# Kernel optimization log

Hardware: AMD Instinct MI355X
Metric: run time of the kernel (lower is better)

The kernel has to match this reference:

```python
import jax, jax.numpy as jnp
import numpy as np

BS, P, MAX_GT, C_IN, NCLS = 16, 4096, 32, 512, 4


def _make_boxes(key, shape):
    k1, k2, k3, k4 = jax.random.split(key, 4)
    x0 = jax.random.uniform(k1, shape) * 500.0
    y0 = jax.random.uniform(k2, shape) * 500.0
    w = 10.0 + jax.random.uniform(k3, shape) * 90.0
    h = 10.0 + jax.random.uniform(k4, shape) * 90.0
    return jnp.stack([x0, y0, x0 + w, y0 + h], -1)


def setup_inputs() -> dict:
    key = jax.random.key(0)
    ks = jax.random.split(key, 10)
    v = jax.random.normal(ks[0], (BS * P, C_IN), jnp.float32)
    rois = _make_boxes(ks[1], (BS, P))
    gt_boxes = _make_boxes(ks[2], (BS, MAX_GT))
    gt_counts = jax.random.randint(ks[3], (BS,), 0, MAX_GT + 1, jnp.int32)
    lab_idx = jax.random.randint(ks[4], (BS,), 0, NCLS)
    labels = jax.nn.one_hot(lab_idx, NCLS, dtype=jnp.float32)
    pre_score = jax.random.uniform(ks[5], (BS, P, NCLS), dtype=jnp.float32)
    cls_w = jax.random.normal(ks[6], (NCLS, C_IN), jnp.float32) * 0.01
    cls_b = jnp.full((NCLS,), -np.log((1.0 - 0.01) / 0.01), jnp.float32)
    reg_w = jax.random.normal(ks[7], (NCLS, C_IN), jnp.float32) * 0.01
    reg_b = jnp.zeros((NCLS,), jnp.float32)
    return {"v": v, "gt_boxes": gt_boxes, "gt_counts": gt_counts, "rois": rois,
            "labels": labels, "pre_score": pre_score, "cls_w": cls_w,
            "cls_b": cls_b, "reg_w": reg_w, "reg_b": reg_b}


def _box_iou(a, b):
    # a: (bs, Na, 4), b: (bs, Nb, 4) -> (bs, Na, Nb)
    area_a = (a[..., 2] - a[..., 0]) * (a[..., 3] - a[..., 1])
    area_b = (b[..., 2] - b[..., 0]) * (b[..., 3] - b[..., 1])
    lt = jnp.maximum(a[..., :, None, :2], b[..., None, :, :2])
    rb = jnp.minimum(a[..., :, None, 2:], b[..., None, :, 2:])
    wh = jnp.clip(rb - lt, 0.0)
    inter = wh[..., 0] * wh[..., 1]
    return inter / (area_a[..., :, None] + area_b[..., None, :] - inter)


def _ce(logits, tgt3):
    # CrossEntropyLoss(reduction='none'): logsumexp - logit[target]
    return jax.nn.logsumexp(logits, -1) - jnp.take_along_axis(logits, tgt3, -1)[..., 0]


def _smooth_l1(x):
    ax = jnp.abs(x)
    return jnp.where(ax < 1.0, 0.5 * ax * ax, ax - 0.5)


def reference(v, gt_boxes, gt_counts, rois, labels, pre_score, cls_w, cls_b, reg_w, reg_b):
    bs, Pn = rois.shape[:2]
    classify = (v @ cls_w.T + cls_b).reshape(bs, Pn, NCLS)
    reg = (v @ reg_w.T + reg_b).reshape(bs, Pn, NCLS)
    label = jnp.argmax(labels, 1)                                  # (bs,)
    lbl3 = jnp.broadcast_to(label[:, None, None], (bs, Pn, 1))

    # background branch: CE on raw logits, mean over proposals
    ce_bg = _ce(classify, lbl3).mean(1)                            # (bs,)

    # foreground branch: CE on clamped logits weighted by pre_score
    c = jnp.clip(classify, 1e-7, 1.0 - 1e-7)
    ps = jnp.take_along_axis(pre_score, lbl3, 2)[..., 0]           # (bs, P)
    ce_fg = _ce(c, lbl3) * ps

    gt_valid = jnp.arange(MAX_GT)[None, :] < gt_counts[:, None]    # (bs, MAX_GT)
    ious = _box_iou(gt_boxes, rois)                                # (bs, MAX_GT, P)
    ious = jnp.where(gt_valid[:, :, None], ious, -1.0)
    mask = jnp.any(ious > 0.5, 1).astype(classify.dtype)           # (bs, P)
    c_fg = (ce_fg * mask).sum(1) / (mask.sum(1) + 1e-7)

    idx = jnp.argmax(ious, 1)                                      # (bs, P)
    g = jnp.take_along_axis(gt_boxes, jnp.broadcast_to(idx[:, :, None], (bs, Pn, 4)), 1)
    gx = (g[..., 2] + g[..., 0]) / 2; gy = (g[..., 3] + g[..., 1]) / 2
    gw = (g[..., 2] - g[..., 0]) / 2; gh = (g[..., 3] - g[..., 1]) / 2
    r = rois
    rx = (r[..., 2] + r[..., 0]) / 2; ry = (r[..., 3] + r[..., 1]) / 2
    rw = (r[..., 2] - r[..., 0]) / 2; rh = (r[..., 3] - r[..., 1]) / 2
    tx = (gx - rx) / (rw + 1e-8); ty = (gy - ry) / (rh + 1e-8)
    tw = jnp.log(gw / (rw + 1e-8)); th = jnp.log(gh / (rh + 1e-8))
    t = jnp.stack([tx, ty, tw, th], -1)                            # (bs, P, 4)
    l1 = (_smooth_l1(reg - t).sum(-1) * mask * ps).sum(1) / (bs * Pn)

    has_gt = gt_counts > 0
    c_list = jnp.where(has_gt, c_fg, 0.0).sum()
    c_bg = jnp.where(has_gt, 0.0, ce_bg).sum()
    bg = jnp.where(has_gt, 0.0, float(Pn)).sum()
    l1_list = jnp.where(has_gt, l1, 0.0).sum()
    return (c_list + c_bg / (bg + 1e-7)) / (bs + 1e-7) + l1_list
```

## Files before the change

kernel.cpp:

```cpp
#include <hip/hip_runtime.h>
#include <math.h>

#define BSZ 16
#define NP 4096
#define MAXGT 32
#define CIN 512
#define NCLS 4

__global__ __launch_bounds__(256) void oicr_main(
    const float* __restrict__ v,
    const float* __restrict__ gt_boxes,
    const int*   __restrict__ gt_counts,
    const float* __restrict__ rois,
    const float* __restrict__ labels,
    const float* __restrict__ pre_score,
    const float* __restrict__ cls_w,
    const float* __restrict__ cls_b,
    const float* __restrict__ reg_w,
    const float* __restrict__ reg_b,
    float* __restrict__ partials)
{
    __shared__ float w8[8][CIN];
    __shared__ float s_bias[8];
    __shared__ float g_x0[MAXGT], g_y0[MAXGT], g_x1[MAXGT], g_y1[MAXGT];
    __shared__ float g_area[MAXGT];
    __shared__ int   g_valid[MAXGT];
    __shared__ int   s_label;
    __shared__ float4 red[256];

    const int tid = threadIdx.x;
    const int b   = blockIdx.x >> 4;
    const int p   = ((blockIdx.x & 15) << 8) + tid;
    const int row = b * NP + p;

    for (int i = tid; i < 8 * CIN; i += 256) {
        int c = i >> 9, k = i & (CIN - 1);
        w8[c][k] = (c < 4) ? cls_w[c * CIN + k] : reg_w[(c - 4) * CIN + k];
    }
    if (tid < 8) s_bias[tid] = (tid < 4) ? cls_b[tid] : reg_b[tid - 4];
    if (tid < MAXGT) {
        int cnt = gt_counts[b];
        const float* g = gt_boxes + (size_t)(b * MAXGT + tid) * 4;
        float x0 = g[0], y0 = g[1], x1 = g[2], y1 = g[3];
        g_x0[tid] = x0; g_y0[tid] = y0; g_x1[tid] = x1; g_y1[tid] = y1;
        g_area[tid] = (x1 - x0) * (y1 - y0);
        g_valid[tid] = (tid < cnt) ? 1 : 0;
    }
    if (tid == 0) {
        const float* L = labels + b * NCLS;
        int bi = 0; float bv = L[0];
        #pragma unroll
        for (int c = 1; c < NCLS; ++c) { if (L[c] > bv) { bv = L[c]; bi = c; } }
        s_label = bi;
    }
    __syncthreads();

    float acc[8];
    #pragma unroll
    for (int c = 0; c < 8; ++c) acc[c] = 0.f;

    const float4* vrow = (const float4*)(v + (size_t)row * CIN);
    #pragma unroll 8
    for (int k4 = 0; k4 < CIN / 4; ++k4) {
        float4 a = vrow[k4];
        const int k = k4 * 4;
        #pragma unroll
        for (int c = 0; c < 8; ++c) {
            float4 wv = *(const float4*)&w8[c][k];
            acc[c] += a.x * wv.x + a.y * wv.y + a.z * wv.z + a.w * wv.w;
        }
    }

    const float cls0 = acc[0] + s_bias[0];
    const float cls1 = acc[1] + s_bias[1];
    const float cls2 = acc[2] + s_bias[2];
    const float cls3 = acc[3] + s_bias[3];
    const float reg0 = acc[4] + s_bias[4];
    const float reg1 = acc[5] + s_bias[5];
    const float reg2 = acc[6] + s_bias[6];
    const float reg3 = acc[7] + s_bias[7];

    const int lbl = s_label;

    float mB = fmaxf(fmaxf(cls0, cls1), fmaxf(cls2, cls3));
    float lseB = mB + logf(expf(cls0 - mB) + expf(cls1 - mB) +
                           expf(cls2 - mB) + expf(cls3 - mB));
    float clsL = (lbl == 0) ? cls0 : (lbl == 1) ? cls1 : (lbl == 2) ? cls2 : cls3;
    float ce_bg = lseB - clsL;

    const float lo = 1e-7f, hi = 1.f - 1e-7f;
    float cc0 = fminf(fmaxf(cls0, lo), hi);
    float cc1 = fminf(fmaxf(cls1, lo), hi);
    float cc2 = fminf(fmaxf(cls2, lo), hi);
    float cc3 = fminf(fmaxf(cls3, lo), hi);
    float mF = fmaxf(fmaxf(cc0, cc1), fmaxf(cc2, cc3));
    float lseF = mF + logf(expf(cc0 - mF) + expf(cc1 - mF) +
                           expf(cc2 - mF) + expf(cc3 - mF));
    float ccL = (lbl == 0) ? cc0 : (lbl == 1) ? cc1 : (lbl == 2) ? cc2 : cc3;
    float ce_fg = lseF - ccL;
    float ps = pre_score[(size_t)row * NCLS + lbl];

    float4 r = *(const float4*)(rois + (size_t)row * 4);
    float rarea = (r.z - r.x) * (r.w - r.y);
    float best = -3.0e38f;
    int   bi = 0;
    int   mk = 0;
    #pragma unroll
    for (int g = 0; g < MAXGT; ++g) {
        float ix0 = fmaxf(r.x, g_x0[g]);
        float iy0 = fmaxf(r.y, g_y0[g]);
        float ix1 = fminf(r.z, g_x1[g]);
        float iy1 = fminf(r.w, g_y1[g]);
        float iw = fmaxf(ix1 - ix0, 0.f);
        float ih = fmaxf(iy1 - iy0, 0.f);
        float inter = iw * ih;
        float iou = inter / (g_area[g] + rarea - inter);
        iou = g_valid[g] ? iou : -1.0f;
        if (iou > best) { best = iou; bi = g; }
        mk |= (iou > 0.5f) ? 1 : 0;
    }
    float maskf = mk ? 1.f : 0.f;

    float gx0 = g_x0[bi], gy0 = g_y0[bi], gx1 = g_x1[bi], gy1 = g_y1[bi];
    float gx = (gx1 + gx0) * 0.5f, gy = (gy1 + gy0) * 0.5f;
    float gw = (gx1 - gx0) * 0.5f, gh = (gy1 - gy0) * 0.5f;
    float rx = (r.z + r.x) * 0.5f, ry = (r.w + r.y) * 0.5f;
    float rw = (r.z - r.x) * 0.5f, rh = (r.w - r.y) * 0.5f;
    float tx = (gx - rx) / (rw + 1e-8f);
    float ty = (gy - ry) / (rh + 1e-8f);
    float tw = logf(gw / (rw + 1e-8f));
    float th = logf(gh / (rh + 1e-8f));

    float d0 = reg0 - tx, d1 = reg1 - ty, d2 = reg2 - tw, d3 = reg3 - th;
    float a0 = fabsf(d0), a1 = fabsf(d1), a2 = fabsf(d2), a3 = fabsf(d3);
    float s0 = (a0 < 1.f) ? 0.5f * a0 * a0 : a0 - 0.5f;
    float s1 = (a1 < 1.f) ? 0.5f * a1 * a1 : a1 - 0.5f;
    float s2 = (a2 < 1.f) ? 0.5f * a2 * a2 : a2 - 0.5f;
    float s3 = (a3 < 1.f) ? 0.5f * a3 * a3 : a3 - 0.5f;
    float sl1 = s0 + s1 + s2 + s3;

    float4 part;
    part.x = ce_bg;
    part.y = ce_fg * ps * maskf;
    part.z = maskf;
    part.w = sl1 * maskf * ps;

    red[tid] = part;
    __syncthreads();
    #pragma unroll
    for (int s = 128; s > 0; s >>= 1) {
        if (tid < s) {
            float4 o = red[tid + s];
            float4 m2 = red[tid];
            m2.x += o.x; m2.y += o.y; m2.z += o.z; m2.w += o.w;
            red[tid] = m2;
        }
        __syncthreads();
    }
    if (tid == 0) {
        float4 t4 = red[0];
        partials[(size_t)blockIdx.x * 4 + 0] = t4.x;
        partials[(size_t)blockIdx.x * 4 + 1] = t4.y;
        partials[(size_t)blockIdx.x * 4 + 2] = t4.z;
        partials[(size_t)blockIdx.x * 4 + 3] = t4.w;
    }
}

__global__ __launch_bounds__(64) void oicr_final(
    const float* __restrict__ partials,
    const int*   __restrict__ gt_counts,
    float* __restrict__ out)
{
    const int lane = threadIdx.x;
    float S0 = 0.f, S1 = 0.f, S2 = 0.f, S3 = 0.f;
    float c_term = 0.f, cbg_term = 0.f, bg_term = 0.f, l1_term = 0.f;
    if (lane < BSZ) {
        for (int blk = 0; blk < 16; ++blk) {
            const float* q = partials + (size_t)(lane * 16 + blk) * 4;
            S0 += q[0]; S1 += q[1]; S2 += q[2]; S3 += q[3];
        }
        bool has = gt_counts[lane] > 0;
        float c_fg       = S1 / (S2 + 1e-7f);
        float ce_bg_mean = S0 / (float)NP;
        float l1b        = S3 / (float)(BSZ * NP);
        c_term   = has ? c_fg : 0.f;
        cbg_term = has ? 0.f : ce_bg_mean;
        bg_term  = has ? 0.f : (float)NP;
        l1_term  = has ? l1b : 0.f;
    }
    #pragma unroll
    for (int off = 32; off > 0; off >>= 1) {
        c_term   += __shfl_down(c_term, off);
        cbg_term += __shfl_down(cbg_term, off);
        bg_term  += __shfl_down(bg_term, off);
        l1_term  += __shfl_down(l1_term, off);
    }
    if (lane == 0) {
        out[0] = (c_term + cbg_term / (bg_term + 1e-7f)) / ((float)BSZ + 1e-7f)
                 + l1_term;
    }
}

extern "C" void kernel_launch(void* const* d_in, const int* in_sizes, int n_in,
                              void* d_out, int out_size, void* d_ws, size_t ws_size,
                              hipStream_t stream)
{
    const float* v         = (const float*)d_in[0];
    const float* gt_boxes  = (const float*)d_in[1];
    const int*   gt_counts = (const int*)  d_in[2];
    const float* rois      = (const float*)d_in[3];
    const float* labels    = (const float*)d_in[4];
    const float* pre_score = (const float*)d_in[5];
    const float* cls_w     = (const float*)d_in[6];
    const float* cls_b     = (const float*)d_in[7];
    const float* reg_w     = (const float*)d_in[8];
    const float* reg_b     = (const float*)d_in[9];
    float* out      = (float*)d_out;
    float* partials = (float*)d_ws;

    oicr_main<<<dim3(256), dim3(256), 0, stream>>>(
        v, gt_boxes, gt_counts, rois, labels, pre_score,
        cls_w, cls_b, reg_w, reg_b, partials);
    oicr_final<<<dim3(1), dim3(64), 0, stream>>>(partials, gt_counts, out);
}
```

Before: 49.10 us.

## Split dot-product K dimension across four waves with 64 rows per block

Each block now handles 64 proposals instead of 256, with the four waves each computing a quarter of the 512-wide dot products and combining them through shared memory. The grid grows from 256 to 1024 blocks, which gives more parallelism on a device with many CUs, and the per-block reduction becomes a single wave shuffle instead of a shared-memory tree. The trade-off is that the 16KB weight tile is reloaded into shared memory by four times as many blocks. The per-thread row access is also strided, so each lane reads a separate 512B slice of its row, which may coalesce poorly.

```diff
diff --git a/kernel.cpp b/kernel.cpp
--- a/kernel.cpp
+++ b/kernel.cpp
@@ -6,8 +6,11 @@
 #define MAXGT 32
 #define CIN 512
 #define NCLS 4
-
-__global__ __launch_bounds__(256) void oicr_main(
+#define PB 64
+#define NBLK (BSZ * NP / PB)
+#define BPB (NP / PB)
+
+__global__ __launch_bounds__(256, 4) void oicr_main(
     const float* __restrict__ v,
     const float* __restrict__ gt_boxes,
     const int*   __restrict__ gt_counts,
@@ -21,18 +24,21 @@
     float* __restrict__ partials)
 {
     __shared__ float w8[8][CIN];
+    __shared__ float red8[4][PB][9];
     __shared__ float s_bias[8];
     __shared__ float g_x0[MAXGT], g_y0[MAXGT], g_x1[MAXGT], g_y1[MAXGT];
     __shared__ float g_area[MAXGT];
     __shared__ int   g_valid[MAXGT];
     __shared__ int   s_label;
-    __shared__ float4 red[256];
-
-    const int tid = threadIdx.x;
-    const int b   = blockIdx.x >> 4;
-    const int p   = ((blockIdx.x & 15) << 8) + tid;
-    const int row = b * NP + p;
-
+
+    const int tid  = threadIdx.x;
+    const int lane = tid & 63;
+    const int wv   = tid >> 6;
+    const int b    = blockIdx.x >> 6;
+    const int p    = (blockIdx.x & 63) * PB + lane;
+    const int row  = b * NP + p;
+
+    #pragma unroll
     for (int i = tid; i < 8 * CIN; i += 256) {
         int c = i >> 9, k = i & (CIN - 1);
         w8[c][k] = (c < 4) ? cls_w[c * CIN + k] : reg_w[(c - 4) * CIN + k];
@@ -55,21 +61,33 @@
     }
     __syncthreads();
 
+    const int kq = __builtin_amdgcn_readfirstlane(wv);
     float acc[8];
     #pragma unroll
     for (int c = 0; c < 8; ++c) acc[c] = 0.f;
 
-    const float4* vrow = (const float4*)(v + (size_t)row * CIN);
+    const float4* vrow = (const float4*)(v + (size_t)row * CIN) + kq * 32;
     #pragma unroll 8
-    for (int k4 = 0; k4 < CIN / 4; ++k4) {
-        float4 a = vrow[k4];
-        const int k = k4 * 4;
+    for (int i = 0; i < 32; ++i) {
+        float4 a = vrow[i];
+        const int k = (kq * 32 + i) * 4;
         #pragma unroll
         for (int c = 0; c < 8; ++c) {
-            float4 wv = *(const float4*)&w8[c][k];
-            acc[c] += a.x * wv.x + a.y * wv.y + a.z * wv.z + a.w * wv.w;
+            float4 w4 = *(const float4*)&w8[c][k];
+            acc[c] += a.x * w4.x + a.y * w4.y + a.z * w4.z + a.w * w4.w;
         }
     }
+
+    #pragma unroll
+    for (int c = 0; c < 8; ++c) red8[wv][lane][c] = acc[c];
+    __syncthreads();
+
+    if (wv != 0) return;
+
+    #pragma unroll
+    for (int c = 0; c < 8; ++c)
+        acc[c] = red8[0][lane][c] + red8[1][lane][c] +
+                 red8[2][lane][c] + red8[3][lane][c];
 
     const float cls0 = acc[0] + s_bias[0];
     const float cls1 = acc[1] + s_bias[1];
@@ -139,30 +157,23 @@
     float s3 = (a3 < 1.f) ? 0.5f * a3 * a3 : a3 - 0.5f;
     float sl1 = s0 + s1 + s2 + s3;
 
-    float4 part;
-    part.x = ce_bg;
-    part.y = ce_fg * ps * maskf;
-    part.z = maskf;
-    part.w = sl1 * maskf * ps;
-
-    red[tid] = part;
-    __syncthreads();
-    #pragma unroll
-    for (int s = 128; s > 0; s >>= 1) {
-        if (tid < s) {
-            float4 o = red[tid + s];
-            float4 m2 = red[tid];
-            m2.x += o.x; m2.y += o.y; m2.z += o.z; m2.w += o.w;
-            red[tid] = m2;
-        }
-        __syncthreads();
-    }
-    if (tid == 0) {
-        float4 t4 = red[0];
-        partials[(size_t)blockIdx.x * 4 + 0] = t4.x;
-        partials[(size_t)blockIdx.x * 4 + 1] = t4.y;
-        partials[(size_t)blockIdx.x * 4 + 2] = t4.z;
-        partials[(size_t)blockIdx.x * 4 + 3] = t4.w;
+    float px = ce_bg;
+    float py = ce_fg * ps * maskf;
+    float pz = maskf;
+    float pw = sl1 * maskf * ps;
+
+    #pragma unroll
+    for (int off = 32; off > 0; off >>= 1) {
+        px += __shfl_down(px, off);
+        py += __shfl_down(py, off);
+        pz += __shfl_down(pz, off);
+        pw += __shfl_down(pw, off);
+    }
+    if (lane == 0) {
+        partials[(size_t)blockIdx.x * 4 + 0] = px;
+        partials[(size_t)blockIdx.x * 4 + 1] = py;
+        partials[(size_t)blockIdx.x * 4 + 2] = pz;
+        partials[(size_t)blockIdx.x * 4 + 3] = pw;
     }
 }
 
@@ -175,8 +186,8 @@
     float S0 = 0.f, S1 = 0.f, S2 = 0.f, S3 = 0.f;
     float c_term = 0.f, cbg_term = 0.f, bg_term = 0.f, l1_term = 0.f;
     if (lane < BSZ) {
-        for (int blk = 0; blk < 16; ++blk) {
-            const float* q = partials + (size_t)(lane * 16 + blk) * 4;
+        for (int blk = 0; blk < BPB; ++blk) {
+            const float* q = partials + (size_t)(lane * BPB + blk) * 4;
             S0 += q[0]; S1 += q[1]; S2 += q[2]; S3 += q[3];
         }
         bool has = gt_counts[lane] > 0;
@@ -218,7 +229,7 @@
     float* out      = (float*)d_out;
     float* partials = (float*)d_ws;
 
-    oicr_main<<<dim3(256), dim3(256), 0, stream>>>(
+    oicr_main<<<dim3(NBLK), dim3(256), 0, stream>>>(
         v, gt_boxes, gt_counts, rois, labels, pre_score,
         cls_w, cls_b, reg_w, reg_b, partials);
     oicr_final<<<dim3(1), dim3(64), 0, stream>>>(partials, gt_counts, out);
```

Result: faster. 46.69 us (-4.9%).

## Coalesce feature loads with wave-per-rows dot products and shuffle transpose-reduce

Applied to the files above, without the earlier changes.

The 8-output GEMV now assigns 32 rows per wavefront, with each lane owning 8 contiguous channels. Every lane loads rows in coalesced 32-byte chunks and keeps its weight slice in registers instead of reading from LDS. Partial dots are combined by a butterfly shuffle reduce-transpose that leaves one (row, output) value per lane, staged in shared memory for the per-row loss epilogue. This removes the strided per-thread row reads of the old layout and doubles the grid to 512 blocks. The cost is heavy register pressure (64 values plus weights) and many shuffles, while only half the threads do the epilogue.

```diff
diff --git a/kernel.cpp b/kernel.cpp
--- a/kernel.cpp
+++ b/kernel.cpp
@@ -6,8 +6,12 @@
 #define MAXGT 32
 #define CIN 512
 #define NCLS 4
-
-__global__ __launch_bounds__(256) void oicr_main(
+#define RPB 128
+#define NBLK (BSZ * NP / RPB)
+#define BPB (NP / RPB)
+#define GRP 4
+
+__global__ __launch_bounds__(256, 2) void oicr_main(
     const float* __restrict__ v,
     const float* __restrict__ gt_boxes,
     const int*   __restrict__ gt_counts,
@@ -20,23 +24,22 @@
     const float* __restrict__ reg_b,
     float* __restrict__ partials)
 {
-    __shared__ float w8[8][CIN];
+    __shared__ float outb[RPB][9];
+    __shared__ float4 red[256];
     __shared__ float s_bias[8];
     __shared__ float g_x0[MAXGT], g_y0[MAXGT], g_x1[MAXGT], g_y1[MAXGT];
     __shared__ float g_area[MAXGT];
     __shared__ int   g_valid[MAXGT];
     __shared__ int   s_label;
-    __shared__ float4 red[256];
-
-    const int tid = threadIdx.x;
-    const int b   = blockIdx.x >> 4;
-    const int p   = ((blockIdx.x & 15) << 8) + tid;
-    const int row = b * NP + p;
-
-    for (int i = tid; i < 8 * CIN; i += 256) {
-        int c = i >> 9, k = i & (CIN - 1);
-        w8[c][k] = (c < 4) ? cls_w[c * CIN + k] : reg_w[(c - 4) * CIN + k];
-    }
+
+    const int tid  = threadIdx.x;
+    const int lane = tid & 63;
+    const int wv   = tid >> 6;
+    const int blk  = blockIdx.x;
+    const int b    = blk >> 5;
+    const int rowblk = blk * RPB;
+    const int wrow   = rowblk + wv * 32;
+
     if (tid < 8) s_bias[tid] = (tid < 4) ? cls_b[tid] : reg_b[tid - 4];
     if (tid < MAXGT) {
         int cnt = gt_counts[b];
@@ -53,99 +56,134 @@
         for (int c = 1; c < NCLS; ++c) { if (L[c] > bv) { bv = L[c]; bi = c; } }
         s_label = bi;
     }
+
+    float4 Wl[8][2];
+    #pragma unroll
+    for (int c = 0; c < 4; ++c) {
+        Wl[c][0]     = *(const float4*)&cls_w[c * CIN + lane * 8];
+        Wl[c][1]     = *(const float4*)&cls_w[c * CIN + lane * 8 + 4];
+        Wl[4 + c][0] = *(const float4*)&reg_w[c * CIN + lane * 8];
+        Wl[4 + c][1] = *(const float4*)&reg_w[c * CIN + lane * 8 + 4];
+    }
+
+    const float4* vb = (const float4*)v + (size_t)wrow * (CIN / 4) + lane * 2;
+
+    for (int g = 0; g < GRP; ++g) {
+        float4 A[8][2];
+        #pragma unroll
+        for (int r = 0; r < 8; ++r) {
+            const float4* p = vb + (size_t)(g * 8 + r) * (CIN / 4);
+            A[r][0] = p[0];
+            A[r][1] = p[1];
+        }
+
+        float val[64];
+        #pragma unroll
+        for (int r = 0; r < 8; ++r) {
+            #pragma unroll
+            for (int c = 0; c < 8; ++c) {
+                float4 a0 = A[r][0], a1 = A[r][1];
+                float4 w0 = Wl[c][0], w1 = Wl[c][1];
+                val[r * 8 + c] = a0.x * w0.x + a0.y * w0.y + a0.z * w0.z + a0.w * w0.w
+                               + a1.x * w1.x + a1.y * w1.y + a1.z * w1.z + a1.w * w1.w;
+            }
+        }
+
+        #pragma unroll
+        for (int s = 0; s < 6; ++s) {
+            const int n = 64 >> s;
+            const int hi = (lane >> s) & 1;
+            #pragma unroll
+            for (int p = 0; p < n; ++p)
+                val[p] += __shfl_xor(val[p], 1 << s, 64);
+            #pragma unroll
+            for (int p2 = 0; p2 < n / 2; ++p2)
+                val[p2] = hi ? val[2 * p2 + 1] : val[2 * p2];
+        }
+
+        outb[wv * 32 + g * 8 + (lane >> 3)][lane & 7] = val[0];
+    }
     __syncthreads();
 
-    float acc[8];
-    #pragma unroll
-    for (int c = 0; c < 8; ++c) acc[c] = 0.f;
-
-    const float4* vrow = (const float4*)(v + (size_t)row * CIN);
-    #pragma unroll 8
-    for (int k4 = 0; k4 < CIN / 4; ++k4) {
-        float4 a = vrow[k4];
-        const int k = k4 * 4;
-        #pragma unroll
-        for (int c = 0; c < 8; ++c) {
-            float4 wv = *(const float4*)&w8[c][k];
-            acc[c] += a.x * wv.x + a.y * wv.y + a.z * wv.z + a.w * wv.w;
-        }
-    }
-
-    const float cls0 = acc[0] + s_bias[0];
-    const float cls1 = acc[1] + s_bias[1];
-    const float cls2 = acc[2] + s_bias[2];
-    const float cls3 = acc[3] + s_bias[3];
-    const float reg0 = acc[4] + s_bias[4];
-    const float reg1 = acc[5] + s_bias[5];
-    const float reg2 = acc[6] + s_bias[6];
-    const float reg3 = acc[7] + s_bias[7];
-
-    const int lbl = s_label;
-
-    float mB = fmaxf(fmaxf(cls0, cls1), fmaxf(cls2, cls3));
-    float lseB = mB + logf(expf(cls0 - mB) + expf(cls1 - mB) +
-                           expf(cls2 - mB) + expf(cls3 - mB));
-    float clsL = (lbl == 0) ? cls0 : (lbl == 1) ? cls1 : (lbl == 2) ? cls2 : cls3;
-    float ce_bg = lseB - clsL;
-
-    const float lo = 1e-7f, hi = 1.f - 1e-7f;
-    float cc0 = fminf(fmaxf(cls0, lo), hi);
-    float cc1 = fminf(fmaxf(cls1, lo), hi);
-    float cc2 = fminf(fmaxf(cls2, lo), hi);
-    float cc3 = fminf(fmaxf(cls3, lo), hi);
-    float mF = fmaxf(fmaxf(cc0, cc1), fmaxf(cc2, cc3));
-    float lseF = mF + logf(expf(cc0 - mF) + expf(cc1 - mF) +
-                           expf(cc2 - mF) + expf(cc3 - mF));
-    float ccL = (lbl == 0) ? cc0 : (lbl == 1) ? cc1 : (lbl == 2) ? cc2 : cc3;
-    float ce_fg = lseF - ccL;
-    float ps = pre_score[(size_t)row * NCLS + lbl];
-
-    float4 r = *(const float4*)(rois + (size_t)row * 4);
-    float rarea = (r.z - r.x) * (r.w - r.y);
-    float best = -3.0e38f;
-    int   bi = 0;
-    int   mk = 0;
-    #pragma unroll
-    for (int g = 0; g < MAXGT; ++g) {
-        float ix0 = fmaxf(r.x, g_x0[g]);
-        float iy0 = fmaxf(r.y, g_y0[g]);
-        float ix1 = fminf(r.z, g_x1[g]);
-        float iy1 = fminf(r.w, g_y1[g]);
-        float iw = fmaxf(ix1 - ix0, 0.f);
-        float ih = fmaxf(iy1 - iy0, 0.f);
-        float inter = iw * ih;
-        float iou = inter / (g_area[g] + rarea - inter);
-        iou = g_valid[g] ? iou : -1.0f;
-        if (iou > best) { best = iou; bi = g; }
-        mk |= (iou > 0.5f) ? 1 : 0;
-    }
-    float maskf = mk ? 1.f : 0.f;
-
-    float gx0 = g_x0[bi], gy0 = g_y0[bi], gx1 = g_x1[bi], gy1 = g_y1[bi];
-    float gx = (gx1 + gx0) * 0.5f, gy = (gy1 + gy0) * 0.5f;
-    float gw = (gx1 - gx0) * 0.5f, gh = (gy1 - gy0) * 0.5f;
-    float rx = (r.z + r.x) * 0.5f, ry = (r.w + r.y) * 0.5f;
-    float rw = (r.z - r.x) * 0.5f, rh = (r.w - r.y) * 0.5f;
-    float tx = (gx - rx) / (rw + 1e-8f);
-    float ty = (gy - ry) / (rh + 1e-8f);
-    float tw = logf(gw / (rw + 1e-8f));
-    float th = logf(gh / (rh + 1e-8f));
-
-    float d0 = reg0 - tx, d1 = reg1 - ty, d2 = reg2 - tw, d3 = reg3 - th;
-    float a0 = fabsf(d0), a1 = fabsf(d1), a2 = fabsf(d2), a3 = fabsf(d3);
-    float s0 = (a0 < 1.f) ? 0.5f * a0 * a0 : a0 - 0.5f;
-    float s1 = (a1 < 1.f) ? 0.5f * a1 * a1 : a1 - 0.5f;
-    float s2 = (a2 < 1.f) ? 0.5f * a2 * a2 : a2 - 0.5f;
-    float s3 = (a3 < 1.f) ? 0.5f * a3 * a3 : a3 - 0.5f;
-    float sl1 = s0 + s1 + s2 + s3;
-
-    float4 part;
-    part.x = ce_bg;
-    part.y = ce_fg * ps * maskf;
-    part.z = maskf;
-    part.w = sl1 * maskf * ps;
-
-    red[tid] = part;
+    float px = 0.f, py = 0.f, pz = 0.f, pw = 0.f;
+    if (tid < RPB) {
+        const int row = rowblk + tid;
+
+        const float cls0 = outb[tid][0] + s_bias[0];
+        const float cls1 = outb[tid][1] + s_bias[1];
+        const float cls2 = outb[tid][2] + s_bias[2];
+        const float cls3 = outb[tid][3] + s_bias[3];
+        const float reg0 = outb[tid][4] + s_bias[4];
+        const float reg1 = outb[tid][5] + s_bias[5];
+        const float reg2 = outb[tid][6] + s_bias[6];
+        const float reg3 = outb[tid][7] + s_bias[7];
+
+        const int lbl = s_label;
+
+        float mB = fmaxf(fmaxf(cls0, cls1), fmaxf(cls2, cls3));
+        float lseB = mB + logf(expf(cls0 - mB) + expf(cls1 - mB) +
+                               expf(cls2 - mB) + expf(cls3 - mB));
+        float clsL = (lbl == 0) ? cls0 : (lbl == 1) ? cls1 : (lbl == 2) ? cls2 : cls3;
+        float ce_bg = lseB - clsL;
+
+        const float lo = 1e-7f, hi2 = 1.f - 1e-7f;
+        float cc0 = fminf(fmaxf(cls0, lo), hi2);
+        float cc1 = fminf(fmaxf(cls1, lo), hi2);
+        float cc2 = fminf(fmaxf(cls2, lo), hi2);
+        float cc3 = fminf(fmaxf(cls3, lo), hi2);
+        float mF = fmaxf(fmaxf(cc0, cc1), fmaxf(cc2, cc3));
+        float lseF = mF + logf(expf(cc0 - mF) + expf(cc1 - mF) +
+                               expf(cc2 - mF) + expf(cc3 - mF));
+        float ccL = (lbl == 0) ? cc0 : (lbl == 1) ? cc1 : (lbl == 2) ? cc2 : cc3;
+        float ce_fg = lseF - ccL;
+        float ps = pre_score[(size_t)row * NCLS + lbl];
+
+        float4 r = *(const float4*)(rois + (size_t)row * 4);
+        float rarea = (r.z - r.x) * (r.w - r.y);
+        float best = -3.0e38f;
+        int   bi = 0;
+        int   mk = 0;
+        #pragma unroll
+        for (int g = 0; g < MAXGT; ++g) {
+            float ix0 = fmaxf(r.x, g_x0[g]);
+            float iy0 = fmaxf(r.y, g_y0[g]);
+            float ix1 = fminf(r.z, g_x1[g]);
+            float iy1 = fminf(r.w, g_y1[g]);
+            float iw = fmaxf(ix1 - ix0, 0.f);
+            float ih = fmaxf(iy1 - iy0, 0.f);
+            float inter = iw * ih;
+            float iou = inter / (g_area[g] + rarea - inter);
+            iou = g_valid[g] ? iou : -1.0f;
+            if (iou > best) { best = iou; bi = g; }
+            mk |= (iou > 0.5f) ? 1 : 0;
+        }
+        float maskf = mk ? 1.f : 0.f;
+
+        float gx0 = g_x0[bi], gy0 = g_y0[bi], gx1 = g_x1[bi], gy1 = g_y1[bi];
+        float gx = (gx1 + gx0) * 0.5f, gy = (gy1 + gy0) * 0.5f;
+        float gw = (gx1 - gx0) * 0.5f, gh = (gy1 - gy0) * 0.5f;
+        float rx = (r.z + r.x) * 0.5f, ry = (r.w + r.y) * 0.5f;
+        float rw = (r.z - r.x) * 0.5f, rh = (r.w - r.y) * 0.5f;
+        float tx = (gx - rx) / (rw + 1e-8f);
+        float ty = (gy - ry) / (rh + 1e-8f);
+        float tw = logf(gw / (rw + 1e-8f));
+        float th = logf(gh / (rh + 1e-8f));
+
+        float d0 = reg0 - tx, d1 = reg1 - ty, d2 = reg2 - tw, d3 = reg3 - th;
+        float a0 = fabsf(d0), a1 = fabsf(d1), a2 = fabsf(d2), a3 = fabsf(d3);
+        float s0 = (a0 < 1.f) ? 0.5f * a0 * a0 : a0 - 0.5f;
+        float s1 = (a1 < 1.f) ? 0.5f * a1 * a1 : a1 - 0.5f;
+        float s2 = (a2 < 1.f) ? 0.5f * a2 * a2 : a2 - 0.5f;
+        float s3 = (a3 < 1.f) ? 0.5f * a3 * a3 : a3 - 0.5f;
+        float sl1 = s0 + s1 + s2 + s3;
+
+        px = ce_bg;
+        py = ce_fg * ps * maskf;
+        pz = maskf;
+        pw = sl1 * maskf * ps;
+    }
+
+    red[tid] = make_float4(px, py, pz, pw);
     __syncthreads();
     #pragma unroll
     for (int s = 128; s > 0; s >>= 1) {
@@ -159,10 +197,10 @@
     }
     if (tid == 0) {
         float4 t4 = red[0];
-        partials[(size_t)blockIdx.x * 4 + 0] = t4.x;
-        partials[(size_t)blockIdx.x * 4 + 1] = t4.y;
-        partials[(size_t)blockIdx.x * 4 + 2] = t4.z;
-        partials[(size_t)blockIdx.x * 4 + 3] = t4.w;
+        partials[(size_t)blk * 4 + 0] = t4.x;
+        partials[(size_t)blk * 4 + 1] = t4.y;
+        partials[(size_t)blk * 4 + 2] = t4.z;
+        partials[(size_t)blk * 4 + 3] = t4.w;
     }
 }
 
@@ -175,8 +213,8 @@
     float S0 = 0.f, S1 = 0.f, S2 = 0.f, S3 = 0.f;
     float c_term = 0.f, cbg_term = 0.f, bg_term = 0.f, l1_term = 0.f;
     if (lane < BSZ) {
-        for (int blk = 0; blk < 16; ++blk) {
-            const float* q = partials + (size_t)(lane * 16 + blk) * 4;
+        for (int blk = 0; blk < BPB; ++blk) {
+            const float* q = partials + (size_t)(lane * BPB + blk) * 4;
             S0 += q[0]; S1 += q[1]; S2 += q[2]; S3 += q[3];
         }
         bool has = gt_counts[lane] > 0;
@@ -218,7 +256,7 @@
     float* out      = (float*)d_out;
     float* partials = (float*)d_ws;
 
-    oicr_main<<<dim3(256), dim3(256), 0, stream>>>(
+    oicr_main<<<dim3(NBLK), dim3(256), 0, stream>>>(
         v, gt_boxes, gt_counts, rois, labels, pre_score,
         cls_w, cls_b, reg_w, reg_b, partials);
     oicr_final<<<dim3(1), dim3(64), 0, stream>>>(partials, gt_counts, out);
```

Result: faster. 43.69 us (-11.0%).
